# Kernel tuning notes

Measured on AMD Instinct MI355X. Metric: run time of the kernel, lower is better.

## Reference

```python
import jax, jax.numpy as jnp
import numpy as np

N = 50000  # num nodes
EPS = 1e-06


def setup_inputs() -> dict:
    key = jax.random.key(0)
    ks = jax.random.split(key, 7)
    E = 800000
    nfeat, nhid, nclass = 64, 128, 64
    x = jax.random.normal(ks[0], (N, nfeat), dtype=jnp.float32)
    src = jax.random.randint(ks[1], (E,), 0, N, dtype=jnp.int32)
    dst = jax.random.randint(ks[2], (E,), 0, N, dtype=jnp.int32)
    W1 = jax.random.normal(ks[3], (nfeat, nhid), dtype=jnp.float32) * (1.0 / np.sqrt(nfeat))
    b1 = jnp.zeros((nhid,), dtype=jnp.float32)
    W2 = jax.random.normal(ks[4], (nhid, nclass), dtype=jnp.float32) * (1.0 / np.sqrt(nhid))
    b2 = jnp.zeros((nclass,), dtype=jnp.float32)
    return {"x": x, "src": src, "dst": dst, "W1": W1, "b1": b1, "W2": W2, "b2": b2}


def _sage_conv(h, src, dst, W, b):
    # spmm(adj, h): sum of neighbor features per destination row
    num = jax.ops.segment_sum(h[src], dst, num_segments=N)  # [N, d]
    # spmm(adj, ones_like(h)): per-row degree broadcast over features
    deg = jax.ops.segment_sum(jnp.ones((src.shape[0],), dtype=h.dtype), dst, num_segments=N)
    neighbor_mean = num / (deg[:, None] + EPS)
    return neighbor_mean @ W + b


def reference(x, src, dst, W1, b1, W2, b2):
    h = jax.nn.relu(_sage_conv(x, src, dst, W1, b1))
    # dropout is identity in eval mode (training=False)
    h = _sage_conv(h, src, dst, W2, b2)
    return jax.nn.log_softmax(h, axis=1)
```

## Files before the change

### kernel.cpp

```cpp
#include <hip/hip_runtime.h>
#include <hip/hip_fp16.h>

#define N_NODES 50000
#define EPS 1e-6f
#define NPAD 50048
#define CAP 64

#define NBKT 512
#define NPB 98
#define NROWS (NBKT * NPB)
#define BCAP 2048
#define CHUNK_A 3072
#define XH8 (N_NODES * 64 / 8)


#define COMP(v, j) ((j) == 0 ? (v).x : (j) == 1 ? (v).y : (j) == 2 ? (v).z : (v).w)

typedef _Float16 half8 __attribute__((ext_vector_type(8)));
typedef float floatx4 __attribute__((ext_vector_type(4)));

__device__ __forceinline__ float4 h4_to_f4(uint2 u) {
  __half2 h0 = *reinterpret_cast<__half2*>(&u.x);
  __half2 h1 = *reinterpret_cast<__half2*>(&u.y);
  float2 f0 = __half22float2(h0);
  float2 f1 = __half22float2(h1);
  float4 r; r.x = f0.x; r.y = f0.y; r.z = f1.x; r.w = f1.y;
  return r;
}

__global__ __launch_bounds__(256) void bucketize_kernel(
    const int* __restrict__ src, const int* __restrict__ dst,
    int* __restrict__ bcur, int* __restrict__ packed,
    const float* __restrict__ x, __half* __restrict__ xh, int E) {
  __shared__ int lcnt[NBKT];
  __shared__ int lbase[NBKT];
  int t = threadIdx.x;

  for (int i = blockIdx.x * 256 + t; i < XH8; i += gridDim.x * 256) {
    float4 a = ((const float4*)x)[2 * i];
    float4 b = ((const float4*)x)[2 * i + 1];
    __half2 h0 = __floats2half2_rn(a.x, a.y);
    __half2 h1 = __floats2half2_rn(a.z, a.w);
    __half2 h2 = __floats2half2_rn(b.x, b.y);
    __half2 h3 = __floats2half2_rn(b.z, b.w);
    uint4 o;
    o.x = *(unsigned int*)&h0; o.y = *(unsigned int*)&h1;
    o.z = *(unsigned int*)&h2; o.w = *(unsigned int*)&h3;
    ((uint4*)xh)[i] = o;
  }

  lcnt[t] = 0; lcnt[t + 256] = 0;
  __syncthreads();
  int base = blockIdx.x * CHUNK_A;
  int end = base + CHUNK_A; if (end > E) end = E;
  for (int e = base + t; e < end; e += 256) atomicAdd(&lcnt[dst[e] / NPB], 1);
  __syncthreads();
  {
    int c0 = lcnt[t], c1 = lcnt[t + 256];
    lbase[t]       = c0 ? atomicAdd(&bcur[t], c0) : 0;
    lbase[t + 256] = c1 ? atomicAdd(&bcur[t + 256], c1) : 0;
    lcnt[t] = 0; lcnt[t + 256] = 0;
  }
  __syncthreads();
  for (int e = base + t; e < end; e += 256) {
    int d = dst[e];
    int b = d / NPB;
    int pos = lbase[b] + atomicAdd(&lcnt[b], 1);
    if (pos < BCAP)
      packed[(b << 11) + pos] = (src[e] << 8) | (d - b * NPB);
  }
}

#define QADD(V0, V1, V2, V3) do {                                         \
    acc.x += ((V0).x + (V1).x) + ((V2).x + (V3).x);                       \
    acc.y += ((V0).y + (V1).y) + ((V2).y + (V3).y);                       \
    acc.z += ((V0).z + (V1).z) + ((V2).z + (V3).z);                       \
    acc.w += ((V0).w + (V1).w) + ((V2).w + (V3).w);                       \
  } while (0)

#define ADD1(V) do {                                                      \
    acc.x += (V).x; acc.y += (V).y; acc.z += (V).z; acc.w += (V).w;       \
  } while (0)

#define GATHER_BODY_H(SRCPTR)                                             \
  do {                                                                    \
    uint2 v[16];                                                          \
    _Pragma("unroll")                                                     \
    for (int j = 0; j < 16; j++)                                          \
      v[j] = ((const uint2*)((SRCPTR) + (size_t)s[j] * 64))[l16];         \
    int rq = rem >> 2, rr = rem & 3;                                      \
    _Pragma("unroll")                                                     \
    for (int q = 0; q < 4; q++) {                                         \
      if (q < rq) {                                                       \
        float4 f0 = h4_to_f4(v[4 * q]);                                   \
        float4 f1 = h4_to_f4(v[4 * q + 1]);                               \
        float4 f2 = h4_to_f4(v[4 * q + 2]);                               \
        float4 f3 = h4_to_f4(v[4 * q + 3]);                               \
        QADD(f0, f1, f2, f3);                                             \
      }                                                                   \
    }                                                                     \
    _Pragma("unroll")                                                     \
    for (int q = 0; q < 4; q++) {                                         \
      if (q == rq && rr > 0) {                                            \
        float4 f0 = h4_to_f4(v[4 * q]);                                   \
        ADD1(f0);                                                         \
        if (rr > 1) { float4 f1 = h4_to_f4(v[4 * q + 1]); ADD1(f1); }     \
        if (rr > 2) { float4 f2 = h4_to_f4(v[4 * q + 2]); ADD1(f2); }     \
      }                                                                   \
    }                                                                     \
  } while (0)

__global__ __launch_bounds__(256) void rows_gather1_kernel(
    const int* __restrict__ bcur, const int* __restrict__ packed,
    int* __restrict__ cnt, int* __restrict__ ssrc,
    const __half* __restrict__ xh, __half* __restrict__ mean1h) {
  __shared__ int lout[NPB * 64];
  __shared__ int lcnt[NPB];
  int t = threadIdx.x;
  int b = blockIdx.x;
  if (t < NPB) lcnt[t] = 0;
  __syncthreads();
  int count = bcur[b]; if (count > BCAP) count = BCAP;
  const int* pk = packed + (b << 11);
  for (int i = t; i < count; i += 256) {
    int p = pk[i];
    int dl = p & 0xff;
    int pos = atomicAdd(&lcnt[dl], 1);
    if (pos < CAP) lout[(dl << 6) + pos] = p >> 8;
  }
  __syncthreads();
  {
    int4* d4 = (int4*)(ssrc + (size_t)b * (NPB * 64));
    const int4* s4 = (const int4*)lout;
    for (int i = t; i < NPB * 16; i += 256) d4[i] = s4[i];
    if (t < NPB) {
      int c = lcnt[t]; if (c > CAP) c = CAP;
      cnt[b * NPB + t] = c;
    }
  }
  int sg = t >> 4;
  int l16 = t & 15;
  for (int dl = sg; dl < NPB; dl += 16) {
    int node = b * NPB + dl;
    if (node >= N_NODES) continue;
    int deg = lcnt[dl]; if (deg > CAP) deg = CAP;
    const int* lrow = &lout[dl << 6];
    float4 acc = {0.f, 0.f, 0.f, 0.f};
    for (int base = 0; base < deg; base += 16) {
      int rem = deg - base; if (rem > 16) rem = 16;
      int s[16];
#pragma unroll
      for (int j = 0; j < 16; j++) s[j] = lrow[base + j];
#pragma unroll
      for (int j = 0; j < 16; j++) { if (j >= rem) s[j] = 0; }
      GATHER_BODY_H(xh);
    }
    float dinv = 1.0f / ((float)deg + EPS);
    __half2 p0 = __floats2half2_rn(acc.x * dinv, acc.y * dinv);
    __half2 p1 = __floats2half2_rn(acc.z * dinv, acc.w * dinv);
    uint2 o;
    o.x = *(unsigned int*)&p0; o.y = *(unsigned int*)&p1;
    ((uint2*)(mean1h + (size_t)node * 64))[l16] = o;
  }
}

__global__ __launch_bounds__(256) void mlp_mfma_kernel(
    const __half* __restrict__ mean1h, const float* __restrict__ W1,
    const float* __restrict__ b1, const float* __restrict__ W2,
    __half* __restrict__ gh) {
  __shared__ __align__(16) char smem[62464];
  __half (*sM)[72]    = (__half(*)[72])smem;
  __half (*sW1T)[72]  = (__half(*)[72])(smem + 9216);
  __half (*sH)[136]   = (__half(*)[136])(smem + 27648);
  __half (*sW2T)[136] = (__half(*)[136])(smem + 45056);
  __half (*sG)[64]    = (__half(*)[64])smem;

  int t = threadIdx.x;
  int row0 = blockIdx.x * 64;

  {
    const uint4* M4 = (const uint4*)(mean1h + (size_t)row0 * 64);
#pragma unroll
    for (int i = 0; i < 2; i++) {
      int idx = t + 256 * i;
      uint4 v = M4[idx];
      *(uint4*)&sM[idx >> 3][(idx & 7) * 8] = v;
    }
  }
#pragma unroll
  for (int i = 0; i < 8; i++) {
    int idx = t + 256 * i;
    int k = idx >> 5, c4 = (idx & 31) * 4;
    float4 w = *(const float4*)(W1 + (size_t)k * 128 + c4);
    sW1T[c4 + 0][k] = __float2half(w.x);
    sW1T[c4 + 1][k] = __float2half(w.y);
    sW1T[c4 + 2][k] = __float2half(w.z);
    sW1T[c4 + 3][k] = __float2half(w.w);
  }
#pragma unroll
  for (int i = 0; i < 8; i++) {
    int idx = t + 256 * i;
    int k = idx >> 4, c4 = (idx & 15) * 4;
    float4 w = *(const float4*)(W2 + (size_t)k * 64 + c4);
    sW2T[c4 + 0][k] = __float2half(w.x);
    sW2T[c4 + 1][k] = __float2half(w.y);
    sW2T[c4 + 2][k] = __float2half(w.z);
    sW2T[c4 + 3][k] = __float2half(w.w);
  }
  __syncthreads();

  int l = t & 63, wv = t >> 6;
  int l16 = l & 15, lg = l >> 4;

  {
    floatx4 acc[4][2];
#pragma unroll
    for (int tc = 0; tc < 2; tc++) {
      float bias = b1[(2 * wv + tc) * 16 + l16];
#pragma unroll
      for (int tr = 0; tr < 4; tr++)
        acc[tr][tc] = (floatx4){bias, bias, bias, bias};
    }
#pragma unroll
    for (int kb = 0; kb < 2; kb++) {
      half8 a[4], bf[2];
#pragma unroll
      for (int tr = 0; tr < 4; tr++)
        a[tr] = *(const half8*)&sM[tr * 16 + l16][kb * 32 + lg * 8];
#pragma unroll
      for (int tc = 0; tc < 2; tc++)
        bf[tc] = *(const half8*)&sW1T[(2 * wv + tc) * 16 + l16][kb * 32 + lg * 8];
#pragma unroll
      for (int tc = 0; tc < 2; tc++)
#pragma unroll
        for (int tr = 0; tr < 4; tr++)
          acc[tr][tc] = __builtin_amdgcn_mfma_f32_16x16x32_f16(
              a[tr], bf[tc], acc[tr][tc], 0, 0, 0);
    }
#pragma unroll
    for (int tc = 0; tc < 2; tc++)
#pragma unroll
      for (int tr = 0; tr < 4; tr++)
#pragma unroll
        for (int r = 0; r < 4; r++) {
          float h = fmaxf(acc[tr][tc][r], 0.f);
          sH[tr * 16 + lg * 4 + r][(2 * wv + tc) * 16 + l16] = __float2half(h);
        }
  }
  __syncthreads();

  {
    floatx4 acc[4];
#pragma unroll
    for (int tc = 0; tc < 4; tc++) acc[tc] = (floatx4){0.f, 0.f, 0.f, 0.f};
    half8 a[4];
#pragma unroll
    for (int kb = 0; kb < 4; kb++)
      a[kb] = *(const half8*)&sH[wv * 16 + l16][kb * 32 + lg * 8];
#pragma unroll
    for (int tc = 0; tc < 4; tc++) {
#pragma unroll
      for (int kb = 0; kb < 4; kb++) {
        half8 bf = *(const half8*)&sW2T[tc * 16 + l16][kb * 32 + lg * 8];
        acc[tc] = __builtin_amdgcn_mfma_f32_16x16x32_f16(a[kb], bf, acc[tc], 0, 0, 0);
      }
    }
#pragma unroll
    for (int tc = 0; tc < 4; tc++)
#pragma unroll
      for (int r = 0; r < 4; r++)
        sG[wv * 16 + lg * 4 + r][tc * 16 + l16] = __float2half(acc[tc][r]);
  }
  __syncthreads();

#pragma unroll
  for (int i = 0; i < 4; i++) {
    int idx = t + 256 * i;
    int row = idx >> 4, c4 = (idx & 15) * 4;
    if (row0 + row < N_NODES)
      *(uint2*)(gh + (size_t)(row0 + row) * 64 + c4) = *(uint2*)&sG[row][c4];
  }
}

__global__ __launch_bounds__(256) void gather2_kernel(
    const __half* __restrict__ gh, const int* __restrict__ cnt,
    const int* __restrict__ ssrc, const float* __restrict__ b2,
    float* __restrict__ out) {
  int t = threadIdx.x;
  int lane = t & 63;
  int sub = lane >> 4;
  int l16 = lane & 15;
  int node = blockIdx.x * 16 + ((t >> 6) << 2) + sub;
  int b = node << 6;
  int e = b + cnt[node];
  float4 acc = {0.f, 0.f, 0.f, 0.f};
  for (int base = b; base < e; base += 16) {
    int rem = e - base; if (rem > 16) rem = 16;
    int s[16];
#pragma unroll
    for (int j = 0; j < 16; j++) s[j] = ssrc[base + j];
#pragma unroll
    for (int j = 0; j < 16; j++) { if (j >= rem) s[j] = 0; }
    GATHER_BODY_H(gh);
  }
  float dinv = 1.0f / ((float)(e - b) + EPS);
  float4 b2v = ((const float4*)b2)[l16];
  float4 val;
  val.x = acc.x * dinv + b2v.x;
  val.y = acc.y * dinv + b2v.y;
  val.z = acc.z * dinv + b2v.z;
  val.w = acc.w * dinv + b2v.w;

  float4 m = val;
#pragma unroll
  for (int o = 8; o > 0; o >>= 1) {
    m.x = fmaxf(m.x, __shfl_xor(m.x, o, 64));
    m.y = fmaxf(m.y, __shfl_xor(m.y, o, 64));
    m.z = fmaxf(m.z, __shfl_xor(m.z, o, 64));
    m.w = fmaxf(m.w, __shfl_xor(m.w, o, 64));
  }
  float mx = fmaxf(fmaxf(m.x, m.z), fmaxf(m.y, m.w));

  float4 ex;
  ex.x = __expf(val.x - mx);
  ex.y = __expf(val.y - mx);
  ex.z = __expf(val.z - mx);
  ex.w = __expf(val.w - mx);
#pragma unroll
  for (int o = 8; o > 0; o >>= 1) {
    ex.x += __shfl_xor(ex.x, o, 64);
    ex.y += __shfl_xor(ex.y, o, 64);
    ex.z += __shfl_xor(ex.z, o, 64);
    ex.w += __shfl_xor(ex.w, o, 64);
  }
  float sm = (ex.x + ex.z) + (ex.y + ex.w);

  float ls = logf(sm);
  float4 o4;
  o4.x = (val.x - mx) - ls;
  o4.y = (val.y - mx) - ls;
  o4.z = (val.z - mx) - ls;
  o4.w = (val.w - mx) - ls;
  ((float4*)(out + (size_t)node * 64))[l16] = o4;
}

extern "C" void kernel_launch(void* const* d_in, const int* in_sizes, int n_in,
                              void* d_out, int out_size, void* d_ws, size_t ws_size,
                              hipStream_t stream) {
  const float* x   = (const float*)d_in[0];
  const int*   src = (const int*)d_in[1];
  const int*   dst = (const int*)d_in[2];
  const float* W1  = (const float*)d_in[3];
  const float* b1  = (const float*)d_in[4];
  const float* W2  = (const float*)d_in[5];
  const float* b2  = (const float*)d_in[6];
  float* out = (float*)d_out;
  int E = in_sizes[1];

  int* bcur   = (int*)d_ws;
  int* packed = bcur + NBKT;
  int* cnt    = packed + (size_t)NBKT * BCAP;
  int* ssrc   = cnt + NROWS;
  __half* mean1h = (__half*)(ssrc + (size_t)NROWS * 64);
  __half* xh   = mean1h + (size_t)NPAD * 64;
  __half* gh   = xh + (size_t)NPAD * 64;

  hipMemsetAsync(bcur, 0, NBKT * sizeof(int), stream);
  bucketize_kernel<<<(E + CHUNK_A - 1) / CHUNK_A, 256, 0, stream>>>(
      src, dst, bcur, packed, x, xh, E);
  rows_gather1_kernel<<<NBKT, 256, 0, stream>>>(bcur, packed, cnt, ssrc, xh, mean1h);
  mlp_mfma_kernel<<<NPAD / 64, 256, 0, stream>>>(mean1h, W1, b1, W2, gh);
  gather2_kernel<<<N_NODES / 16, 256, 0, stream>>>(gh, cnt, ssrc, b2, out);
}
```

Before: 159.0 us.

## Split second-layer gather into two column-half passes for cache locality

```diff
diff --git a/kernel.cpp b/kernel.cpp
--- a/kernel.cpp
+++ b/kernel.cpp
@@ -26,6 +26,11 @@
   float2 f1 = __half22float2(h1);
   float4 r; r.x = f0.x; r.y = f0.y; r.z = f1.x; r.w = f1.y;
   return r;
+}
+
+__device__ __forceinline__ float2 h2_to_f2(unsigned int u) {
+  __half2 h = *reinterpret_cast<__half2*>(&u);
+  return __half22float2(h);
 }
 
 __global__ __launch_bounds__(256) void bucketize_kernel(
@@ -82,6 +87,13 @@
     acc.x += (V).x; acc.y += (V).y; acc.z += (V).z; acc.w += (V).w;       \
   } while (0)
 
+#define QADD2(F0, F1, F2, F3) do {                                        \
+    acc.x += ((F0).x + (F1).x) + ((F2).x + (F3).x);                       \
+    acc.y += ((F0).y + (F1).y) + ((F2).y + (F3).y);                       \
+  } while (0)
+
+#define ADD1_2(F) do { acc.x += (F).x; acc.y += (F).y; } while (0)
+
 #define GATHER_BODY_H(SRCPTR)                                             \
   do {                                                                    \
     uint2 v[16];                                                          \
@@ -106,6 +118,34 @@
         ADD1(f0);                                                         \
         if (rr > 1) { float4 f1 = h4_to_f4(v[4 * q + 1]); ADD1(f1); }     \
         if (rr > 2) { float4 f2 = h4_to_f4(v[4 * q + 2]); ADD1(f2); }     \
+      }                                                                   \
+    }                                                                     \
+  } while (0)
+
+#define GATHER_BODY_H2(SRCPTR, HOFF)                                      \
+  do {                                                                    \
+    unsigned int v[16];                                                   \
+    _Pragma("unroll")                                                     \
+    for (int j = 0; j < 16; j++)                                          \
+      v[j] = ((const unsigned int*)((SRCPTR) + (size_t)s[j] * 64 + (HOFF)))[l16]; \
+    int rq = rem >> 2, rr = rem & 3;                                      \
+    _Pragma("unroll")                                                     \
+    for (int q = 0; q < 4; q++) {                                         \
+      if (q < rq) {                                                       \
+        float2 f0 = h2_to_f2(v[4 * q]);                                   \
+        float2 f1 = h2_to_f2(v[4 * q + 1]);                               \
+        float2 f2 = h2_to_f2(v[4 * q + 2]);                               \
+        float2 f3 = h2_to_f2(v[4 * q + 3]);                               \
+        QADD2(f0, f1, f2, f3);                                            \
+      }                                                                   \
+    }                                                                     \
+    _Pragma("unroll")                                                     \
+    for (int q = 0; q < 4; q++) {                                         \
+      if (q == rq && rr > 0) {                                            \
+        float2 f0 = h2_to_f2(v[4 * q]);                                   \
+        ADD1_2(f0);                                                       \
+        if (rr > 1) { float2 f1 = h2_to_f2(v[4 * q + 1]); ADD1_2(f1); }   \
+        if (rr > 2) { float2 f2 = h2_to_f2(v[4 * q + 2]); ADD1_2(f2); }   \
       }                                                                   \
     }                                                                     \
   } while (0)
@@ -282,10 +322,10 @@
   }
 }
 
-__global__ __launch_bounds__(256) void gather2_kernel(
+__global__ __launch_bounds__(256) void gather2a_kernel(
     const __half* __restrict__ gh, const int* __restrict__ cnt,
     const int* __restrict__ ssrc, const float* __restrict__ b2,
-    float* __restrict__ out) {
+    float* __restrict__ valA) {
   int t = threadIdx.x;
   int lane = t & 63;
   int sub = lane >> 4;
@@ -293,7 +333,7 @@
   int node = blockIdx.x * 16 + ((t >> 6) << 2) + sub;
   int b = node << 6;
   int e = b + cnt[node];
-  float4 acc = {0.f, 0.f, 0.f, 0.f};
+  float2 acc = {0.f, 0.f};
   for (int base = b; base < e; base += 16) {
     int rem = e - base; if (rem > 16) rem = 16;
     int s[16];
@@ -301,15 +341,44 @@
     for (int j = 0; j < 16; j++) s[j] = ssrc[base + j];
 #pragma unroll
     for (int j = 0; j < 16; j++) { if (j >= rem) s[j] = 0; }
-    GATHER_BODY_H(gh);
+    GATHER_BODY_H2(gh, 0);
   }
   float dinv = 1.0f / ((float)(e - b) + EPS);
-  float4 b2v = ((const float4*)b2)[l16];
-  float4 val;
+  float2 b2v = *(const float2*)(b2 + l16 * 2);
+  float2 val;
   val.x = acc.x * dinv + b2v.x;
   val.y = acc.y * dinv + b2v.y;
-  val.z = acc.z * dinv + b2v.z;
-  val.w = acc.w * dinv + b2v.w;
+  ((float2*)(valA + (size_t)node * 32))[l16] = val;
+}
+
+__global__ __launch_bounds__(256) void gather2b_kernel(
+    const __half* __restrict__ gh, const int* __restrict__ cnt,
+    const int* __restrict__ ssrc, const float* __restrict__ b2,
+    const float* __restrict__ valA, float* __restrict__ out) {
+  int t = threadIdx.x;
+  int lane = t & 63;
+  int sub = lane >> 4;
+  int l16 = lane & 15;
+  int node = blockIdx.x * 16 + ((t >> 6) << 2) + sub;
+  int b = node << 6;
+  int e = b + cnt[node];
+  float2 acc = {0.f, 0.f};
+  for (int base = b; base < e; base += 16) {
+    int rem = e - base; if (rem > 16) rem = 16;
+    int s[16];
+#pragma unroll
+    for (int j = 0; j < 16; j++) s[j] = ssrc[base + j];
+#pragma unroll
+    for (int j = 0; j < 16; j++) { if (j >= rem) s[j] = 0; }
+    GATHER_BODY_H2(gh, 32);
+  }
+  float dinv = 1.0f / ((float)(e - b) + EPS);
+  float2 b2v = *(const float2*)(b2 + 32 + l16 * 2);
+  float2 own;
+  own.x = acc.x * dinv + b2v.x;
+  own.y = acc.y * dinv + b2v.y;
+  float2 pA = ((const float2*)(valA + (size_t)node * 32))[l16];
+  float4 val; val.x = pA.x; val.y = pA.y; val.z = own.x; val.w = own.y;
 
   float4 m = val;
 #pragma unroll
@@ -336,12 +405,13 @@
   float sm = (ex.x + ex.z) + (ex.y + ex.w);
 
   float ls = logf(sm);
-  float4 o4;
-  o4.x = (val.x - mx) - ls;
-  o4.y = (val.y - mx) - ls;
-  o4.z = (val.z - mx) - ls;
-  o4.w = (val.w - mx) - ls;
-  ((float4*)(out + (size_t)node * 64))[l16] = o4;
+  float2 o0, o1;
+  o0.x = (val.x - mx) - ls;
+  o0.y = (val.y - mx) - ls;
+  o1.x = (val.z - mx) - ls;
+  o1.y = (val.w - mx) - ls;
+  ((float2*)(out + (size_t)node * 64))[l16] = o0;
+  ((float2*)(out + (size_t)node * 64 + 32))[l16] = o1;
 }
 
 extern "C" void kernel_launch(void* const* d_in, const int* in_sizes, int n_in,
@@ -364,11 +434,13 @@
   __half* mean1h = (__half*)(ssrc + (size_t)NROWS * 64);
   __half* xh   = mean1h + (size_t)NPAD * 64;
   __half* gh   = xh + (size_t)NPAD * 64;
+  float* valA  = (float*)(gh + (size_t)NPAD * 64);
 
   hipMemsetAsync(bcur, 0, NBKT * sizeof(int), stream);
   bucketize_kernel<<<(E + CHUNK_A - 1) / CHUNK_A, 256, 0, stream>>>(
       src, dst, bcur, packed, x, xh, E);
   rows_gather1_kernel<<<NBKT, 256, 0, stream>>>(bcur, packed, cnt, ssrc, xh, mean1h);
   mlp_mfma_kernel<<<NPAD / 64, 256, 0, stream>>>(mean1h, W1, b1, W2, gh);
-  gather2_kernel<<<N_NODES / 16, 256, 0, stream>>>(gh, cnt, ssrc, b2, out);
-}
+  gather2a_kernel<<<N_NODES / 16, 256, 0, stream>>>(gh, cnt, ssrc, b2, valA);
+  gather2b_kernel<<<N_NODES / 16, 256, 0, stream>>>(gh, cnt, ssrc, b2, valA, out);
+}
```

Result: slower. 169.3 us (+6.5%).
